# Optimization experiments

Hardware: AMD Instinct MI355X
Metric: run time of the kernel (lower is better)

Reference implementation:

```python
import jax, jax.numpy as jnp
import numpy as np
import math

N_ANGLES = 8
HIGH_FREQ_RATIO = 0.3


def setup_inputs() -> dict:
    key = jax.random.key(0)
    k1, k2 = jax.random.split(key)
    x = jax.random.normal(k1, (4, 256, 256, 256), dtype=jnp.float32)
    # learnable per-angle weights, init near enhance_init=1.0 with small perturbation
    angle_weights = 1.0 + 0.1 * jax.random.normal(k2, (N_ANGLES,), dtype=jnp.float32)
    return {"x": x, "angle_weights": angle_weights}


def _angle_gain(H, W, angle_weights):
    # Build [H, W] real gain: angle-sector weight in the high-frequency band, 1 elsewhere.
    cy, cx = H // 2, W // 2
    y = jnp.arange(H, dtype=jnp.float32)[:, None] - cy
    x = jnp.arange(W, dtype=jnp.float32)[None, :] - cx
    r = jnp.sqrt(y * y + x * x)
    theta = jnp.arctan2(y, x) + math.pi  # [0, 2*pi]
    angle_step = 2.0 * math.pi / N_ANGLES
    angle_idx = jnp.mod(jnp.floor(theta / angle_step).astype(jnp.int32), N_ANGLES)
    r_max = min(cy, cx)
    high_freq_mask = r > HIGH_FREQ_RATIO * r_max
    weights = angle_weights[angle_idx]  # [H, W]
    return jnp.where(high_freq_mask, weights, jnp.ones_like(weights))


def reference(x, angle_weights):
    # x: [B, C, H, W]
    H, W = x.shape[-2], x.shape[-1]
    gain = _angle_gain(H, W, angle_weights)  # [H, W], real
    xf = jnp.fft.fftshift(jnp.fft.fft2(x, norm="ortho"), axes=(-2, -1))
    # mag*gain * exp(i*phase) == gain * (mag*exp(i*phase)) == gain * spectrum (gain real)
    xf_enh = xf * gain
    x_enh = jnp.fft.ifft2(jnp.fft.ifftshift(xf_enh, axes=(-2, -1)), norm="ortho").real
    return x + x_enh
```

## Files before the change

### kernel.cpp

```cpp
#include <hip/hip_runtime.h>
#include <math.h>

#define PI_F 3.14159265358979323846f
#define WSYNC() asm volatile("s_waitcnt lgkmcnt(0)" ::: "memory")

__device__ __forceinline__ float2 cmul(float2 a, float2 b) {
    return make_float2(a.x * b.x - a.y * b.y, a.x * b.y + a.y * b.x);
}
__device__ __forceinline__ float2 cmulc(float2 a, float2 b) {
    return make_float2(a.x * b.x + a.y * b.y, a.y * b.x - a.x * b.y);
}
__device__ __forceinline__ int digitrev4(int p) {
    return ((p & 3) << 6) | (((p >> 2) & 3) << 4) | (((p >> 4) & 3) << 2) | ((p >> 6) & 3);
}
__device__ __forceinline__ void tw3(int eu, float2& w1, float2& w2, float2& w3) {
    float sn, cs;
    __sincosf(-(2.0f * PI_F / 256.0f) * (float)eu, &sn, &cs);
    w1 = make_float2(cs, sn);
    w2 = cmul(w1, w1);
    w3 = cmul(w2, w1);
}

template<int S>
__device__ __forceinline__ void stage_fwd_j(float2* line, int j, float2 w1, float2 w2, float2 w3) {
    const int h = 1 << (2 * S);
    int k  = j & (h - 1);
    int i0 = ((j >> (2 * S)) << (2 * S + 2)) + k;
    float2 a0 = line[i0], a1 = line[i0 + h], a2 = line[i0 + 2 * h], a3 = line[i0 + 3 * h];
    float2 t0 = make_float2(a0.x + a2.x, a0.y + a2.y);
    float2 t1 = make_float2(a0.x - a2.x, a0.y - a2.y);
    float2 t2 = make_float2(a1.x + a3.x, a1.y + a3.y);
    float2 u  = make_float2(a1.x - a3.x, a1.y - a3.y);
    float2 t3 = make_float2(u.y, -u.x);
    line[i0]         = make_float2(t0.x + t2.x, t0.y + t2.y);
    line[i0 + h]     = cmul(make_float2(t1.x + t3.x, t1.y + t3.y), w1);
    line[i0 + 2 * h] = cmul(make_float2(t0.x - t2.x, t0.y - t2.y), w2);
    line[i0 + 3 * h] = cmul(make_float2(t1.x - t3.x, t1.y - t3.y), w3);
}
template<int S>
__device__ __forceinline__ void stage_inv_j(float2* line, int j, float2 w1, float2 w2, float2 w3) {
    const int h = 1 << (2 * S);
    int k  = j & (h - 1);
    int i0 = ((j >> (2 * S)) << (2 * S + 2)) + k;
    float2 b0 = line[i0];
    float2 b1 = cmulc(line[i0 + h], w1);
    float2 b2 = cmulc(line[i0 + 2 * h], w2);
    float2 b3 = cmulc(line[i0 + 3 * h], w3);
    float2 t0 = make_float2(b0.x + b2.x, b0.y + b2.y);
    float2 t1 = make_float2(b0.x - b2.x, b0.y - b2.y);
    float2 t2 = make_float2(b1.x + b3.x, b1.y + b3.y);
    float2 u  = make_float2(b1.x - b3.x, b1.y - b3.y);
    float2 t3 = make_float2(-u.y, u.x);
    line[i0]         = make_float2(t0.x + t2.x, t0.y + t2.y);
    line[i0 + h]     = make_float2(t1.x + t3.x, t1.y + t3.y);
    line[i0 + 2 * h] = make_float2(t0.x - t2.x, t0.y - t2.y);
    line[i0 + 3 * h] = make_float2(t1.x - t3.x, t1.y - t3.y);
}

__device__ __forceinline__ float gain1(float fy, float fx, const float* sw) {
    float r2 = fy * fy + fx * fx;
    float theta = atan2f(fy, fx) + PI_F;
    int idx = ((int)floorf(theta * (4.0f / PI_F))) & 7;
    float wv = sw[idx];
    return (r2 > 1474.56f) ? wv : 1.0f;
}

__global__ __launch_bounds__(256) void k_gain_lut(const float* __restrict__ wts, float* __restrict__ lut2) {
    __shared__ float sw[8];
    int h = threadIdx.x, w = blockIdx.x;
    if (h < 8) sw[h] = wts[h];
    __syncthreads();
    int kw = digitrev4(w), kh = digitrev4(h);
    float fx  = (kw < 128) ? (float)kw : (float)(kw - 256);
    float fx2 = (kw == 128) ? -128.0f : -fx;
    float fy  = (kh < 128) ? (float)kh : (float)(kh - 256);
    float fy2 = (kh == 128) ? -128.0f : -fy;
    float g1 = gain1(fy, fx, sw);
    float g2 = gain1(fy2, fx2, sw);
    lut2[w * 256 + h] = (1.0f + 0.5f * (g1 + g2)) * (1.0f / 65536.0f);
}

__global__ __launch_bounds__(256) void k_row_fwd(const float* __restrict__ x, float* __restrict__ out) {
    __shared__ float2 lds[8][256];
    int t = threadIdx.x, wv = t >> 6, lane = t & 63;
    int gr = blockIdx.x * 8 + wv * 2;
    int q = gr >> 8, h = gr & 255;
    int plane = ((q >> 7) << 8) + ((q & 127) << 1);
    size_t rA = ((size_t)plane << 16) + ((size_t)h << 8);
    size_t rB = rA + 65536;
    float2* L0 = lds[wv * 2];
    float2* L1 = lds[wv * 2 + 1];
    int w = lane * 4;
    float4 re0 = *(const float4*)(x + rA + w);
    float4 im0 = *(const float4*)(x + rB + w);
    float4 re1 = *(const float4*)(x + rA + 256 + w);
    float4 im1 = *(const float4*)(x + rB + 256 + w);
    *(float4*)&L0[w]     = make_float4(re0.x, im0.x, re0.y, im0.y);
    *(float4*)&L0[w + 2] = make_float4(re0.z, im0.z, re0.w, im0.w);
    *(float4*)&L1[w]     = make_float4(re1.x, im1.x, re1.y, im1.y);
    *(float4*)&L1[w + 2] = make_float4(re1.z, im1.z, re1.w, im1.w);
    WSYNC();
    { float2 w1,w2,w3; tw3((lane & 63) << 0, w1,w2,w3);
      stage_fwd_j<3>(L0, lane, w1,w2,w3); stage_fwd_j<3>(L1, lane, w1,w2,w3); WSYNC(); }
    { float2 w1,w2,w3; tw3((lane & 15) << 2, w1,w2,w3);
      stage_fwd_j<2>(L0, lane, w1,w2,w3); stage_fwd_j<2>(L1, lane, w1,w2,w3); WSYNC(); }
    { float2 w1,w2,w3; tw3((lane & 3) << 4, w1,w2,w3);
      stage_fwd_j<1>(L0, lane, w1,w2,w3); stage_fwd_j<1>(L1, lane, w1,w2,w3); WSYNC(); }
    { float2 one = make_float2(1.0f, 0.0f);
      stage_fwd_j<0>(L0, lane, one,one,one); stage_fwd_j<0>(L1, lane, one,one,one); WSYNC(); }
    float4 a0 = *(float4*)&L0[w], a1 = *(float4*)&L0[w + 2];
    float4 b0 = *(float4*)&L1[w], b1 = *(float4*)&L1[w + 2];
    *(float4*)(out + rA + w)       = make_float4(a0.x, a0.z, a1.x, a1.z);
    *(float4*)(out + rB + w)       = make_float4(a0.y, a0.w, a1.y, a1.w);
    *(float4*)(out + rA + 256 + w) = make_float4(b0.x, b0.z, b1.x, b1.z);
    *(float4*)(out + rB + 256 + w) = make_float4(b0.y, b0.w, b1.y, b1.w);
}

template<int S>
__device__ __forceinline__ void col_stage_fwd(float2* line, int jb) {
#pragma unroll
    for (int i2 = 0; i2 < 4; ++i2) {
        int j = jb + 16 * i2;
        int k = j & ((1 << (2 * S)) - 1);
        float2 w1,w2,w3; tw3(k << (6 - 2 * S), w1,w2,w3);
        stage_fwd_j<S>(line, j, w1,w2,w3);
    }
}
template<int S>
__device__ __forceinline__ void col_stage_inv(float2* line, int jb) {
#pragma unroll
    for (int i2 = 0; i2 < 4; ++i2) {
        int j = jb + 16 * i2;
        int k = j & ((1 << (2 * S)) - 1);
        float2 w1,w2,w3; tw3(k << (6 - 2 * S), w1,w2,w3);
        stage_inv_j<S>(line, j, w1,w2,w3);
    }
}

template<bool USE_LUT>
__global__ __launch_bounds__(256) void k_col(float* __restrict__ data,
                                            const float* __restrict__ lut2,
                                            const float* __restrict__ wts) {
    __shared__ float2 tile[16][258];
    __shared__ float sw[8];
    int t = threadIdx.x;
    if (!USE_LUT && t < 8) sw[t] = wts[t];
    int q = blockIdx.x >> 4, wt = blockIdx.x & 15, w0 = wt * 16;
    int plane = ((q >> 7) << 8) + ((q & 127) << 1);
    size_t baseA = ((size_t)plane << 16) + (size_t)w0;
    size_t baseB = baseA + 65536;
    int c0 = (t & 3) * 4, h0 = (t >> 2) * 4;
    {
        float4 reR[4], imR[4];
#pragma unroll
        for (int r = 0; r < 4; ++r) {
            reR[r] = *(const float4*)(data + baseA + (size_t)(h0 + r) * 256 + c0);
            imR[r] = *(const float4*)(data + baseB + (size_t)(h0 + r) * 256 + c0);
        }
#pragma unroll
        for (int k = 0; k < 4; ++k) {
            float r0 = (&reR[0].x)[k], i0v = (&imR[0].x)[k];
            float r1 = (&reR[1].x)[k], i1v = (&imR[1].x)[k];
            float r2 = (&reR[2].x)[k], i2v = (&imR[2].x)[k];
            float r3 = (&reR[3].x)[k], i3v = (&imR[3].x)[k];
            *(float4*)&tile[c0 + k][h0]     = make_float4(r0, i0v, r1, i1v);
            *(float4*)&tile[c0 + k][h0 + 2] = make_float4(r2, i2v, r3, i3v);
        }
    }
    __syncthreads();
    int wv = t >> 6, lane = t & 63;
    int col = wv * 4 + (lane & 3);
    int jb  = lane >> 2;
    float2* line = tile[col];
    col_stage_fwd<3>(line, jb); WSYNC();
    col_stage_fwd<2>(line, jb); WSYNC();
    col_stage_fwd<1>(line, jb); WSYNC();
    col_stage_fwd<0>(line, jb); WSYNC();
    {
        int hb = jb * 16;
        if (USE_LUT) {
            const float* lp = lut2 + (size_t)(w0 + col) * 256 + hb;
#pragma unroll
            for (int ch = 0; ch < 4; ++ch) {
                float4 s4 = *(const float4*)(lp + ch * 4);
#pragma unroll
                for (int e = 0; e < 4; ++e) {
                    int hh = hb + ch * 4 + e;
                    float sc = (&s4.x)[e];
                    float2 v = line[hh];
                    line[hh] = make_float2(v.x * sc, v.y * sc);
                }
            }
        } else {
            int kw = digitrev4(w0 + col);
            float fx  = (kw < 128) ? (float)kw : (float)(kw - 256);
            float fx2 = (kw == 128) ? -128.0f : -fx;
#pragma unroll
            for (int m = 0; m < 16; ++m) {
                int hh = hb + m;
                int kh = digitrev4(hh);
                float fy  = (kh < 128) ? (float)kh : (float)(kh - 256);
                float fy2 = (kh == 128) ? -128.0f : -fy;
                float g1 = gain1(fy, fx, sw);
                float g2 = gain1(fy2, fx2, sw);
                float sc = (1.0f + 0.5f * (g1 + g2)) * (1.0f / 65536.0f);
                float2 v = line[hh];
                line[hh] = make_float2(v.x * sc, v.y * sc);
            }
        }
        WSYNC();
    }
    col_stage_inv<0>(line, jb); WSYNC();
    col_stage_inv<1>(line, jb); WSYNC();
    col_stage_inv<2>(line, jb); WSYNC();
    col_stage_inv<3>(line, jb); WSYNC();
    __syncthreads();
    {
        float2 v[4][4];
#pragma unroll
        for (int k = 0; k < 4; ++k) {
            float4 lo = *(float4*)&tile[c0 + k][h0];
            float4 hi = *(float4*)&tile[c0 + k][h0 + 2];
            v[k][0] = make_float2(lo.x, lo.y);
            v[k][1] = make_float2(lo.z, lo.w);
            v[k][2] = make_float2(hi.x, hi.y);
            v[k][3] = make_float2(hi.z, hi.w);
        }
#pragma unroll
        for (int r = 0; r < 4; ++r) {
            *(float4*)(data + baseA + (size_t)(h0 + r) * 256 + c0) =
                make_float4(v[0][r].x, v[1][r].x, v[2][r].x, v[3][r].x);
            *(float4*)(data + baseB + (size_t)(h0 + r) * 256 + c0) =
                make_float4(v[0][r].y, v[1][r].y, v[2][r].y, v[3][r].y);
        }
    }
}

__global__ __launch_bounds__(256) void k_row_inv(float* __restrict__ data) {
    __shared__ float2 lds[8][256];
    int t = threadIdx.x, wv = t >> 6, lane = t & 63;
    int gr = blockIdx.x * 8 + wv * 2;
    int q = gr >> 8, h = gr & 255;
    int plane = ((q >> 7) << 8) + ((q & 127) << 1);
    size_t rA = ((size_t)plane << 16) + ((size_t)h << 8);
    size_t rB = rA + 65536;
    float2* L0 = lds[wv * 2];
    float2* L1 = lds[wv * 2 + 1];
    int w = lane * 4;
    float4 re0 = *(const float4*)(data + rA + w);
    float4 im0 = *(const float4*)(data + rB + w);
    float4 re1 = *(const float4*)(data + rA + 256 + w);
    float4 im1 = *(const float4*)(data + rB + 256 + w);
    *(float4*)&L0[w]     = make_float4(re0.x, im0.x, re0.y, im0.y);
    *(float4*)&L0[w + 2] = make_float4(re0.z, im0.z, re0.w, im0.w);
    *(float4*)&L1[w]     = make_float4(re1.x, im1.x, re1.y, im1.y);
    *(float4*)&L1[w + 2] = make_float4(re1.z, im1.z, re1.w, im1.w);
    WSYNC();
    { float2 one = make_float2(1.0f, 0.0f);
      stage_inv_j<0>(L0, lane, one,one,one); stage_inv_j<0>(L1, lane, one,one,one); WSYNC(); }
    { float2 w1,w2,w3; tw3((lane & 3) << 4, w1,w2,w3);
      stage_inv_j<1>(L0, lane, w1,w2,w3); stage_inv_j<1>(L1, lane, w1,w2,w3); WSYNC(); }
    { float2 w1,w2,w3; tw3((lane & 15) << 2, w1,w2,w3);
      stage_inv_j<2>(L0, lane, w1,w2,w3); stage_inv_j<2>(L1, lane, w1,w2,w3); WSYNC(); }
    { float2 w1,w2,w3; tw3((lane & 63) << 0, w1,w2,w3);
      stage_inv_j<3>(L0, lane, w1,w2,w3); stage_inv_j<3>(L1, lane, w1,w2,w3); WSYNC(); }
    float4 a0 = *(float4*)&L0[w], a1 = *(float4*)&L0[w + 2];
    float4 b0 = *(float4*)&L1[w], b1 = *(float4*)&L1[w + 2];
    *(float4*)(data + rA + w)       = make_float4(a0.x, a0.z, a1.x, a1.z);
    *(float4*)(data + rB + w)       = make_float4(a0.y, a0.w, a1.y, a1.w);
    *(float4*)(data + rA + 256 + w) = make_float4(b0.x, b0.z, b1.x, b1.z);
    *(float4*)(data + rB + 256 + w) = make_float4(b0.y, b0.w, b1.y, b1.w);
}

extern "C" void kernel_launch(void* const* d_in, const int* in_sizes, int n_in,
                              void* d_out, int out_size, void* d_ws, size_t ws_size,
                              hipStream_t stream) {
    const float* x   = (const float*)d_in[0];
    const float* wts = (const float*)d_in[1];
    float* out = (float*)d_out;
    (void)in_sizes; (void)n_in; (void)out_size;
    bool use_lut = (ws_size >= 256 * 256 * sizeof(float)) && (d_ws != nullptr);
    if (use_lut) {
        k_gain_lut<<<256, 256, 0, stream>>>(wts, (float*)d_ws);
    }
    k_row_fwd<<<16384, 256, 0, stream>>>(x, out);
    if (use_lut) {
        k_col<true><<<8192, 256, 0, stream>>>(out, (const float*)d_ws, wts);
    } else {
        k_col<false><<<8192, 256, 0, stream>>>(out, nullptr, wts);
    }
    k_row_inv<<<16384, 256, 0, stream>>>(out);
}
```

Before: 657.2 us.

## Swizzle LDS FFT layout, fuse last/first radix-4 stages in registers, hoist twiddles

Applies an XOR swizzle to every LDS index in the row and column FFT kernels to cut bank conflicts. The last forward and first inverse radix-4 stages now run in registers: in the row kernels they are fused with the global store/load, and in the column kernel they are fused with the gain multiply, removing several LDS round trips and syncs. Twiddles are computed once per thread instead of per stage or per column. The column kernel also changes how work maps to threads (one wavefront handles 4 columns in 2 pairs, lane = butterfly), which drops the tile padding and adds scalar LDS accesses and more register pressure.

After: 650.3 us. Within noise of the previous version (-1.1%).

```diff
diff --git a/kernel.cpp b/kernel.cpp
--- a/kernel.cpp
+++ b/kernel.cpp
@@ -13,6 +13,8 @@
 __device__ __forceinline__ int digitrev4(int p) {
     return ((p & 3) << 6) | (((p >> 2) & 3) << 4) | (((p >> 4) & 3) << 2) | ((p >> 6) & 3);
 }
+__device__ __forceinline__ int SW(int i) { return i ^ ((i >> 4) & 15); }
+
 __device__ __forceinline__ void tw3(int eu, float2& w1, float2& w2, float2& w3) {
     float sn, cs;
     __sincosf(-(2.0f * PI_F / 256.0f) * (float)eu, &sn, &cs);
@@ -21,40 +23,58 @@
     w3 = cmul(w2, w1);
 }
 
+__device__ __forceinline__ void bfly4_fwd(float2 a0, float2 a1, float2 a2, float2 a3,
+                                          float2& o0, float2& o1, float2& o2, float2& o3) {
+    float2 t0 = make_float2(a0.x + a2.x, a0.y + a2.y);
+    float2 t1 = make_float2(a0.x - a2.x, a0.y - a2.y);
+    float2 t2 = make_float2(a1.x + a3.x, a1.y + a3.y);
+    float2 u  = make_float2(a1.x - a3.x, a1.y - a3.y);
+    float2 t3 = make_float2(u.y, -u.x);
+    o0 = make_float2(t0.x + t2.x, t0.y + t2.y);
+    o1 = make_float2(t1.x + t3.x, t1.y + t3.y);
+    o2 = make_float2(t0.x - t2.x, t0.y - t2.y);
+    o3 = make_float2(t1.x - t3.x, t1.y - t3.y);
+}
+__device__ __forceinline__ void bfly4_inv(float2 a0, float2 a1, float2 a2, float2 a3,
+                                          float2& o0, float2& o1, float2& o2, float2& o3) {
+    float2 t0 = make_float2(a0.x + a2.x, a0.y + a2.y);
+    float2 t1 = make_float2(a0.x - a2.x, a0.y - a2.y);
+    float2 t2 = make_float2(a1.x + a3.x, a1.y + a3.y);
+    float2 u  = make_float2(a1.x - a3.x, a1.y - a3.y);
+    float2 t3 = make_float2(-u.y, u.x);
+    o0 = make_float2(t0.x + t2.x, t0.y + t2.y);
+    o1 = make_float2(t1.x + t3.x, t1.y + t3.y);
+    o2 = make_float2(t0.x - t2.x, t0.y - t2.y);
+    o3 = make_float2(t1.x - t3.x, t1.y - t3.y);
+}
+
 template<int S>
 __device__ __forceinline__ void stage_fwd_j(float2* line, int j, float2 w1, float2 w2, float2 w3) {
     const int h = 1 << (2 * S);
     int k  = j & (h - 1);
     int i0 = ((j >> (2 * S)) << (2 * S + 2)) + k;
-    float2 a0 = line[i0], a1 = line[i0 + h], a2 = line[i0 + 2 * h], a3 = line[i0 + 3 * h];
-    float2 t0 = make_float2(a0.x + a2.x, a0.y + a2.y);
-    float2 t1 = make_float2(a0.x - a2.x, a0.y - a2.y);
-    float2 t2 = make_float2(a1.x + a3.x, a1.y + a3.y);
-    float2 u  = make_float2(a1.x - a3.x, a1.y - a3.y);
-    float2 t3 = make_float2(u.y, -u.x);
-    line[i0]         = make_float2(t0.x + t2.x, t0.y + t2.y);
-    line[i0 + h]     = cmul(make_float2(t1.x + t3.x, t1.y + t3.y), w1);
-    line[i0 + 2 * h] = cmul(make_float2(t0.x - t2.x, t0.y - t2.y), w2);
-    line[i0 + 3 * h] = cmul(make_float2(t1.x - t3.x, t1.y - t3.y), w3);
+    int p0 = SW(i0), p1 = SW(i0 + h), p2 = SW(i0 + 2 * h), p3 = SW(i0 + 3 * h);
+    float2 a0 = line[p0], a1 = line[p1], a2 = line[p2], a3 = line[p3];
+    float2 o0, o1, o2, o3;
+    bfly4_fwd(a0, a1, a2, a3, o0, o1, o2, o3);
+    line[p0] = o0;
+    line[p1] = cmul(o1, w1);
+    line[p2] = cmul(o2, w2);
+    line[p3] = cmul(o3, w3);
 }
 template<int S>
 __device__ __forceinline__ void stage_inv_j(float2* line, int j, float2 w1, float2 w2, float2 w3) {
     const int h = 1 << (2 * S);
     int k  = j & (h - 1);
     int i0 = ((j >> (2 * S)) << (2 * S + 2)) + k;
-    float2 b0 = line[i0];
-    float2 b1 = cmulc(line[i0 + h], w1);
-    float2 b2 = cmulc(line[i0 + 2 * h], w2);
-    float2 b3 = cmulc(line[i0 + 3 * h], w3);
-    float2 t0 = make_float2(b0.x + b2.x, b0.y + b2.y);
-    float2 t1 = make_float2(b0.x - b2.x, b0.y - b2.y);
-    float2 t2 = make_float2(b1.x + b3.x, b1.y + b3.y);
-    float2 u  = make_float2(b1.x - b3.x, b1.y - b3.y);
-    float2 t3 = make_float2(-u.y, u.x);
-    line[i0]         = make_float2(t0.x + t2.x, t0.y + t2.y);
-    line[i0 + h]     = make_float2(t1.x + t3.x, t1.y + t3.y);
-    line[i0 + 2 * h] = make_float2(t0.x - t2.x, t0.y - t2.y);
-    line[i0 + 3 * h] = make_float2(t1.x - t3.x, t1.y - t3.y);
+    int p0 = SW(i0), p1 = SW(i0 + h), p2 = SW(i0 + 2 * h), p3 = SW(i0 + 3 * h);
+    float2 b0 = line[p0];
+    float2 b1 = cmulc(line[p1], w1);
+    float2 b2 = cmulc(line[p2], w2);
+    float2 b3 = cmulc(line[p3], w3);
+    float2 o0, o1, o2, o3;
+    bfly4_inv(b0, b1, b2, b3, o0, o1, o2, o3);
+    line[p0] = o0; line[p1] = o1; line[p2] = o2; line[p3] = o3;
 }
 
 __device__ __forceinline__ float gain1(float fy, float fx, const float* sw) {
@@ -95,61 +115,73 @@
     float4 im0 = *(const float4*)(x + rB + w);
     float4 re1 = *(const float4*)(x + rA + 256 + w);
     float4 im1 = *(const float4*)(x + rB + 256 + w);
-    *(float4*)&L0[w]     = make_float4(re0.x, im0.x, re0.y, im0.y);
-    *(float4*)&L0[w + 2] = make_float4(re0.z, im0.z, re0.w, im0.w);
-    *(float4*)&L1[w]     = make_float4(re1.x, im1.x, re1.y, im1.y);
-    *(float4*)&L1[w + 2] = make_float4(re1.z, im1.z, re1.w, im1.w);
+    float2 w31, w32, w33, w21, w22, w23, w11, w12, w13;
+    tw3(lane,             w31, w32, w33);
+    tw3((lane & 15) << 2, w21, w22, w23);
+    tw3((lane & 3)  << 4, w11, w12, w13);
+    int s0 = SW(w), s1 = SW(w + 1), s2 = SW(w + 2), s3 = SW(w + 3);
+    L0[s0] = make_float2(re0.x, im0.x); L0[s1] = make_float2(re0.y, im0.y);
+    L0[s2] = make_float2(re0.z, im0.z); L0[s3] = make_float2(re0.w, im0.w);
+    L1[s0] = make_float2(re1.x, im1.x); L1[s1] = make_float2(re1.y, im1.y);
+    L1[s2] = make_float2(re1.z, im1.z); L1[s3] = make_float2(re1.w, im1.w);
     WSYNC();
-    { float2 w1,w2,w3; tw3((lane & 63) << 0, w1,w2,w3);
-      stage_fwd_j<3>(L0, lane, w1,w2,w3); stage_fwd_j<3>(L1, lane, w1,w2,w3); WSYNC(); }
-    { float2 w1,w2,w3; tw3((lane & 15) << 2, w1,w2,w3);
-      stage_fwd_j<2>(L0, lane, w1,w2,w3); stage_fwd_j<2>(L1, lane, w1,w2,w3); WSYNC(); }
-    { float2 w1,w2,w3; tw3((lane & 3) << 4, w1,w2,w3);
-      stage_fwd_j<1>(L0, lane, w1,w2,w3); stage_fwd_j<1>(L1, lane, w1,w2,w3); WSYNC(); }
-    { float2 one = make_float2(1.0f, 0.0f);
-      stage_fwd_j<0>(L0, lane, one,one,one); stage_fwd_j<0>(L1, lane, one,one,one); WSYNC(); }
-    float4 a0 = *(float4*)&L0[w], a1 = *(float4*)&L0[w + 2];
-    float4 b0 = *(float4*)&L1[w], b1 = *(float4*)&L1[w + 2];
-    *(float4*)(out + rA + w)       = make_float4(a0.x, a0.z, a1.x, a1.z);
-    *(float4*)(out + rB + w)       = make_float4(a0.y, a0.w, a1.y, a1.w);
-    *(float4*)(out + rA + 256 + w) = make_float4(b0.x, b0.z, b1.x, b1.z);
-    *(float4*)(out + rB + 256 + w) = make_float4(b0.y, b0.w, b1.y, b1.w);
-}
-
-template<int S>
-__device__ __forceinline__ void col_stage_fwd(float2* line, int jb) {
-#pragma unroll
-    for (int i2 = 0; i2 < 4; ++i2) {
-        int j = jb + 16 * i2;
-        int k = j & ((1 << (2 * S)) - 1);
-        float2 w1,w2,w3; tw3(k << (6 - 2 * S), w1,w2,w3);
-        stage_fwd_j<S>(line, j, w1,w2,w3);
-    }
-}
-template<int S>
-__device__ __forceinline__ void col_stage_inv(float2* line, int jb) {
-#pragma unroll
-    for (int i2 = 0; i2 < 4; ++i2) {
-        int j = jb + 16 * i2;
-        int k = j & ((1 << (2 * S)) - 1);
-        float2 w1,w2,w3; tw3(k << (6 - 2 * S), w1,w2,w3);
-        stage_inv_j<S>(line, j, w1,w2,w3);
+    stage_fwd_j<3>(L0, lane, w31, w32, w33); stage_fwd_j<3>(L1, lane, w31, w32, w33); WSYNC();
+    stage_fwd_j<2>(L0, lane, w21, w22, w23); stage_fwd_j<2>(L1, lane, w21, w22, w23); WSYNC();
+    stage_fwd_j<1>(L0, lane, w11, w12, w13); stage_fwd_j<1>(L1, lane, w11, w12, w13); WSYNC();
+    {
+        float2 o0, o1, o2, o3;
+        bfly4_fwd(L0[s0], L0[s1], L0[s2], L0[s3], o0, o1, o2, o3);
+        *(float4*)(out + rA + w) = make_float4(o0.x, o1.x, o2.x, o3.x);
+        *(float4*)(out + rB + w) = make_float4(o0.y, o1.y, o2.y, o3.y);
+        bfly4_fwd(L1[s0], L1[s1], L1[s2], L1[s3], o0, o1, o2, o3);
+        *(float4*)(out + rA + 256 + w) = make_float4(o0.x, o1.x, o2.x, o3.x);
+        *(float4*)(out + rB + 256 + w) = make_float4(o0.y, o1.y, o2.y, o3.y);
     }
 }
 
 template<bool USE_LUT>
 __global__ __launch_bounds__(256) void k_col(float* __restrict__ data,
-                                            const float* __restrict__ lut2,
-                                            const float* __restrict__ wts) {
-    __shared__ float2 tile[16][258];
-    __shared__ float sw[8];
+                                             const float* __restrict__ lut2,
+                                             const float* __restrict__ wts) {
+    __shared__ float2 tile[16][256];
     int t = threadIdx.x;
-    if (!USE_LUT && t < 8) sw[t] = wts[t];
     int q = blockIdx.x >> 4, wt = blockIdx.x & 15, w0 = wt * 16;
     int plane = ((q >> 7) << 8) + ((q & 127) << 1);
     size_t baseA = ((size_t)plane << 16) + (size_t)w0;
     size_t baseB = baseA + 65536;
     int c0 = (t & 3) * 4, h0 = (t >> 2) * 4;
+    int wv = t >> 6, lane = t & 63;
+    int i0 = lane * 4;
+
+    float4 gAr[2], gBr[2];
+    if (!USE_LUT) {
+        if (t < 8) ((float*)tile)[t] = wts[t];
+        __syncthreads();
+        const float* swp = (const float*)tile;
+#pragma unroll
+        for (int cp = 0; cp < 2; ++cp) {
+#pragma unroll
+            for (int cc = 0; cc < 2; ++cc) {
+                int col = wv * 4 + cp * 2 + cc;
+                int kw = digitrev4(w0 + col);
+                float fx  = (kw < 128) ? (float)kw : (float)(kw - 256);
+                float fx2 = (kw == 128) ? -128.0f : -fx;
+                float4 g;
+#pragma unroll
+                for (int d = 0; d < 4; ++d) {
+                    int kh = digitrev4(i0 + d);
+                    float fy  = (kh < 128) ? (float)kh : (float)(kh - 256);
+                    float fy2 = (kh == 128) ? -128.0f : -fy;
+                    float g1v = gain1(fy, fx, swp);
+                    float g2v = gain1(fy2, fx2, swp);
+                    (&g.x)[d] = (1.0f + 0.5f * (g1v + g2v)) * (1.0f / 65536.0f);
+                }
+                if (cc == 0) gAr[cp] = g; else gBr[cp] = g;
+            }
+        }
+        __syncthreads();
+    }
+
     {
         float4 reR[4], imR[4];
 #pragma unroll
@@ -158,80 +190,63 @@
             imR[r] = *(const float4*)(data + baseB + (size_t)(h0 + r) * 256 + c0);
         }
 #pragma unroll
-        for (int k = 0; k < 4; ++k) {
-            float r0 = (&reR[0].x)[k], i0v = (&imR[0].x)[k];
-            float r1 = (&reR[1].x)[k], i1v = (&imR[1].x)[k];
-            float r2 = (&reR[2].x)[k], i2v = (&imR[2].x)[k];
-            float r3 = (&reR[3].x)[k], i3v = (&imR[3].x)[k];
-            *(float4*)&tile[c0 + k][h0]     = make_float4(r0, i0v, r1, i1v);
-            *(float4*)&tile[c0 + k][h0 + 2] = make_float4(r2, i2v, r3, i3v);
+        for (int r = 0; r < 4; ++r) {
+            int p = SW(h0 + r);
+#pragma unroll
+            for (int k = 0; k < 4; ++k)
+                tile[c0 + k][p] = make_float2((&reR[r].x)[k], (&imR[r].x)[k]);
         }
     }
     __syncthreads();
-    int wv = t >> 6, lane = t & 63;
-    int col = wv * 4 + (lane & 3);
-    int jb  = lane >> 2;
-    float2* line = tile[col];
-    col_stage_fwd<3>(line, jb); WSYNC();
-    col_stage_fwd<2>(line, jb); WSYNC();
-    col_stage_fwd<1>(line, jb); WSYNC();
-    col_stage_fwd<0>(line, jb); WSYNC();
+
+    float2 w31, w32, w33, w21, w22, w23, w11, w12, w13;
+    tw3(lane,             w31, w32, w33);
+    tw3((lane & 15) << 2, w21, w22, w23);
+    tw3((lane & 3)  << 4, w11, w12, w13);
+    int p0 = SW(i0), p1 = SW(i0 + 1), p2 = SW(i0 + 2), p3 = SW(i0 + 3);
+#pragma unroll
+    for (int cp = 0; cp < 2; ++cp) {
+        int colA = wv * 4 + cp * 2, colB = colA + 1;
+        float2* LA = tile[colA];
+        float2* LB = tile[colB];
+        float4 gA, gB;
+        if (USE_LUT) {
+            gA = *(const float4*)(lut2 + (size_t)(w0 + colA) * 256 + i0);
+            gB = *(const float4*)(lut2 + (size_t)(w0 + colB) * 256 + i0);
+        } else {
+            gA = gAr[cp]; gB = gBr[cp];
+        }
+        stage_fwd_j<3>(LA, lane, w31, w32, w33); stage_fwd_j<3>(LB, lane, w31, w32, w33); WSYNC();
+        stage_fwd_j<2>(LA, lane, w21, w22, w23); stage_fwd_j<2>(LB, lane, w21, w22, w23); WSYNC();
+        stage_fwd_j<1>(LA, lane, w11, w12, w13); stage_fwd_j<1>(LB, lane, w11, w12, w13); WSYNC();
+        {
+            float2 o0, o1, o2, o3, r0, r1, r2, r3;
+            bfly4_fwd(LA[p0], LA[p1], LA[p2], LA[p3], o0, o1, o2, o3);
+            o0.x *= gA.x; o0.y *= gA.x; o1.x *= gA.y; o1.y *= gA.y;
+            o2.x *= gA.z; o2.y *= gA.z; o3.x *= gA.w; o3.y *= gA.w;
+            bfly4_inv(o0, o1, o2, o3, r0, r1, r2, r3);
+            LA[p0] = r0; LA[p1] = r1; LA[p2] = r2; LA[p3] = r3;
+            bfly4_fwd(LB[p0], LB[p1], LB[p2], LB[p3], o0, o1, o2, o3);
+            o0.x *= gB.x; o0.y *= gB.x; o1.x *= gB.y; o1.y *= gB.y;
+            o2.x *= gB.z; o2.y *= gB.z; o3.x *= gB.w; o3.y *= gB.w;
+            bfly4_inv(o0, o1, o2, o3, r0, r1, r2, r3);
+            LB[p0] = r0; LB[p1] = r1; LB[p2] = r2; LB[p3] = r3;
+        }
+        WSYNC();
+        stage_inv_j<1>(LA, lane, w11, w12, w13); stage_inv_j<1>(LB, lane, w11, w12, w13); WSYNC();
+        stage_inv_j<2>(LA, lane, w21, w22, w23); stage_inv_j<2>(LB, lane, w21, w22, w23); WSYNC();
+        stage_inv_j<3>(LA, lane, w31, w32, w33); stage_inv_j<3>(LB, lane, w31, w32, w33); WSYNC();
+    }
+    __syncthreads();
+
     {
-        int hb = jb * 16;
-        if (USE_LUT) {
-            const float* lp = lut2 + (size_t)(w0 + col) * 256 + hb;
-#pragma unroll
-            for (int ch = 0; ch < 4; ++ch) {
-                float4 s4 = *(const float4*)(lp + ch * 4);
-#pragma unroll
-                for (int e = 0; e < 4; ++e) {
-                    int hh = hb + ch * 4 + e;
-                    float sc = (&s4.x)[e];
-                    float2 v = line[hh];
-                    line[hh] = make_float2(v.x * sc, v.y * sc);
-                }
-            }
-        } else {
-            int kw = digitrev4(w0 + col);
-            float fx  = (kw < 128) ? (float)kw : (float)(kw - 256);
-            float fx2 = (kw == 128) ? -128.0f : -fx;
-#pragma unroll
-            for (int m = 0; m < 16; ++m) {
-                int hh = hb + m;
-                int kh = digitrev4(hh);
-                float fy  = (kh < 128) ? (float)kh : (float)(kh - 256);
-                float fy2 = (kh == 128) ? -128.0f : -fy;
-                float g1 = gain1(fy, fx, sw);
-                float g2 = gain1(fy2, fx2, sw);
-                float sc = (1.0f + 0.5f * (g1 + g2)) * (1.0f / 65536.0f);
-                float2 v = line[hh];
-                line[hh] = make_float2(v.x * sc, v.y * sc);
-            }
-        }
-        WSYNC();
-    }
-    col_stage_inv<0>(line, jb); WSYNC();
-    col_stage_inv<1>(line, jb); WSYNC();
-    col_stage_inv<2>(line, jb); WSYNC();
-    col_stage_inv<3>(line, jb); WSYNC();
-    __syncthreads();
-    {
-        float2 v[4][4];
-#pragma unroll
-        for (int k = 0; k < 4; ++k) {
-            float4 lo = *(float4*)&tile[c0 + k][h0];
-            float4 hi = *(float4*)&tile[c0 + k][h0 + 2];
-            v[k][0] = make_float2(lo.x, lo.y);
-            v[k][1] = make_float2(lo.z, lo.w);
-            v[k][2] = make_float2(hi.x, hi.y);
-            v[k][3] = make_float2(hi.z, hi.w);
-        }
 #pragma unroll
         for (int r = 0; r < 4; ++r) {
-            *(float4*)(data + baseA + (size_t)(h0 + r) * 256 + c0) =
-                make_float4(v[0][r].x, v[1][r].x, v[2][r].x, v[3][r].x);
-            *(float4*)(data + baseB + (size_t)(h0 + r) * 256 + c0) =
-                make_float4(v[0][r].y, v[1][r].y, v[2][r].y, v[3][r].y);
+            int p = SW(h0 + r);
+            float2 v0 = tile[c0 + 0][p], v1 = tile[c0 + 1][p];
+            float2 v2 = tile[c0 + 2][p], v3 = tile[c0 + 3][p];
+            *(float4*)(data + baseA + (size_t)(h0 + r) * 256 + c0) = make_float4(v0.x, v1.x, v2.x, v3.x);
+            *(float4*)(data + baseB + (size_t)(h0 + r) * 256 + c0) = make_float4(v0.y, v1.y, v2.y, v3.y);
         }
     }
 }
@@ -251,25 +266,30 @@
     float4 im0 = *(const float4*)(data + rB + w);
     float4 re1 = *(const float4*)(data + rA + 256 + w);
     float4 im1 = *(const float4*)(data + rB + 256 + w);
-    *(float4*)&L0[w]     = make_float4(re0.x, im0.x, re0.y, im0.y);
-    *(float4*)&L0[w + 2] = make_float4(re0.z, im0.z, re0.w, im0.w);
-    *(float4*)&L1[w]     = make_float4(re1.x, im1.x, re1.y, im1.y);
-    *(float4*)&L1[w + 2] = make_float4(re1.z, im1.z, re1.w, im1.w);
+    float2 w31, w32, w33, w21, w22, w23, w11, w12, w13;
+    tw3(lane,             w31, w32, w33);
+    tw3((lane & 15) << 2, w21, w22, w23);
+    tw3((lane & 3)  << 4, w11, w12, w13);
+    int s0 = SW(w), s1 = SW(w + 1), s2 = SW(w + 2), s3 = SW(w + 3);
+    {
+        float2 o0, o1, o2, o3;
+        bfly4_inv(make_float2(re0.x, im0.x), make_float2(re0.y, im0.y),
+                  make_float2(re0.z, im0.z), make_float2(re0.w, im0.w), o0, o1, o2, o3);
+        L0[s0] = o0; L0[s1] = o1; L0[s2] = o2; L0[s3] = o3;
+        bfly4_inv(make_float2(re1.x, im1.x), make_float2(re1.y, im1.y),
+                  make_float2(re1.z, im1.z), make_float2(re1.w, im1.w), o0, o1, o2, o3);
+        L1[s0] = o0; L1[s1] = o1; L1[s2] = o2; L1[s3] = o3;
+    }
     WSYNC();
-    { float2 one = make_float2(1.0f, 0.0f);
-      stage_inv_j<0>(L0, lane, one,one,one); stage_inv_j<0>(L1, lane, one,one,one); WSYNC(); }
-    { float2 w1,w2,w3; tw3((lane & 3) << 4, w1,w2,w3);
-      stage_inv_j<1>(L0, lane, w1,w2,w3); stage_inv_j<1>(L1, lane, w1,w2,w3); WSYNC(); }
-    { float2 w1,w2,w3; tw3((lane & 15) << 2, w1,w2,w3);
-      stage_inv_j<2>(L0, lane, w1,w2,w3); stage_inv_j<2>(L1, lane, w1,w2,w3); WSYNC(); }
-    { float2 w1,w2,w3; tw3((lane & 63) << 0, w1,w2,w3);
-      stage_inv_j<3>(L0, lane, w1,w2,w3); stage_inv_j<3>(L1, lane, w1,w2,w3); WSYNC(); }
-    float4 a0 = *(float4*)&L0[w], a1 = *(float4*)&L0[w + 2];
-    float4 b0 = *(float4*)&L1[w], b1 = *(float4*)&L1[w + 2];
-    *(float4*)(data + rA + w)       = make_float4(a0.x, a0.z, a1.x, a1.z);
-    *(float4*)(data + rB + w)       = make_float4(a0.y, a0.w, a1.y, a1.w);
-    *(float4*)(data + rA + 256 + w) = make_float4(b0.x, b0.z, b1.x, b1.z);
-    *(float4*)(data + rB + 256 + w) = make_float4(b0.y, b0.w, b1.y, b1.w);
+    stage_inv_j<1>(L0, lane, w11, w12, w13); stage_inv_j<1>(L1, lane, w11, w12, w13); WSYNC();
+    stage_inv_j<2>(L0, lane, w21, w22, w23); stage_inv_j<2>(L1, lane, w21, w22, w23); WSYNC();
+    stage_inv_j<3>(L0, lane, w31, w32, w33); stage_inv_j<3>(L1, lane, w31, w32, w33); WSYNC();
+    float2 a0 = L0[s0], a1 = L0[s1], a2 = L0[s2], a3 = L0[s3];
+    float2 b0 = L1[s0], b1 = L1[s1], b2 = L1[s2], b3 = L1[s3];
+    *(float4*)(data + rA + w)       = make_float4(a0.x, a1.x, a2.x, a3.x);
+    *(float4*)(data + rB + w)       = make_float4(a0.y, a1.y, a2.y, a3.y);
+    *(float4*)(data + rA + 256 + w) = make_float4(b0.x, b1.x, b2.x, b3.x);
+    *(float4*)(data + rB + 256 + w) = make_float4(b0.y, b1.y, b2.y, b3.y);
 }
 
 extern "C" void kernel_launch(void* const* d_in, const int* in_sizes, int n_in,
```
